# Kernel tuning notes

Measured on AMD Instinct MI355X. Metric: run time of the kernel, lower is better.

Reference implementation:

```python
import jax, jax.numpy as jnp
import numpy as np
from jax import lax

NUM_CAMERAS = 15
INPUT_SIZE = 1024
NUM_TIMESTEPS = 60
BATCH = 256


def setup_inputs() -> dict:
    key = jax.random.key(0)
    k1, k2, k3, k4, k5, k6 = jax.random.split(key, 6)
    H = INPUT_SIZE
    s = 1.0 / np.sqrt(H)  # PyTorch RNNCell init: U(-1/sqrt(H), 1/sqrt(H))
    x = jax.random.normal(k1, (BATCH, H), dtype=jnp.float32)
    cam = jax.random.randint(k2, (BATCH,), 0, NUM_CAMERAS)
    # per-camera GRUCell params, PyTorch layout: gates [r, z, n] stacked -> 3H
    W_ih = jax.random.uniform(k3, (NUM_CAMERAS, 3 * H, H), jnp.float32, -s, s)
    W_hh = jax.random.uniform(k4, (NUM_CAMERAS, 3 * H, H), jnp.float32, -s, s)
    b_ih = jax.random.uniform(k5, (NUM_CAMERAS, 3 * H), jnp.float32, -s, s)
    b_hh = jax.random.uniform(k6, (NUM_CAMERAS, 3 * H), jnp.float32, -s, s)
    return {"x": x, "cam": cam, "W_ih": W_ih, "W_hh": W_hh, "b_ih": b_ih, "b_hh": b_hh}


def reference(x, cam, W_ih, W_hh, b_ih, b_hh):
    B, H = x.shape
    rows = jnp.arange(B)
    # input projection is constant across timesteps (same x fed every step):
    # compute for all cameras as one GEMM, then gather each sample's camera.
    gi_all = jnp.einsum('bh,cgh->bcg', x, W_ih) + b_ih[None]  # [B,C,3H]
    gi = gi_all[rows, cam]                                     # [B,3H]
    gi_r, gi_z, gi_n = jnp.split(gi, 3, axis=1)
    bhh = b_hh[cam]                                            # [B,3H]

    def step(h, _):
        gh_all = jnp.einsum('bh,cgh->bcg', h, W_hh)            # [B,C,3H] GEMM
        gh = gh_all[rows, cam] + bhh                           # [B,3H]
        gh_r, gh_z, gh_n = jnp.split(gh, 3, axis=1)
        r = jax.nn.sigmoid(gi_r + gh_r)
        z = jax.nn.sigmoid(gi_z + gh_z)
        n = jnp.tanh(gi_n + r * gh_n)
        h_new = (1.0 - z) * n + z * h
        return h_new, h_new

    h0 = jnp.zeros((B, H), dtype=x.dtype)
    _, hs = lax.scan(step, h0, None, length=NUM_TIMESTEPS)     # [T,B,H]
    return jnp.transpose(hs, (1, 2, 0))                        # [B,H,T]
```

## Files before the change

### kernel.cpp

```cpp
#include <hip/hip_runtime.h>
#include <math.h>

#define HD 1024
#define BB 256
#define NCAM 15
#define TT 60
#define G3 3072
#define LDW 36
#define NS 24
#define TCH 20

typedef _Float16 f16x8 __attribute__((ext_vector_type(8)));
typedef float f32x4 __attribute__((ext_vector_type(4)));

__device__ __forceinline__ unsigned short f2h(float f) {
    _Float16 h = (_Float16)f;
    unsigned short u;
    __builtin_memcpy(&u, &h, 2);
    return u;
}
__device__ __forceinline__ float sigf(float v) { return 1.f / (1.f + expf(-v)); }

__device__ __forceinline__ void dma16(const void* g, void* l) {
    __builtin_amdgcn_global_load_lds(
        (const __attribute__((address_space(1))) unsigned int*)g,
        (__attribute__((address_space(3))) unsigned int*)l, 16, 0, 0);
}

__global__ void group_kernel(const int* __restrict__ cam,
                             int* __restrict__ off, int* __restrict__ list) {
    __shared__ int cnt[NCAM];
    __shared__ int soff[NCAM + 1];
    int tid = threadIdx.x;
    if (tid < NCAM) cnt[tid] = 0;
    __syncthreads();
    int c = cam[tid];
    int pos = atomicAdd(&cnt[c], 1);
    __syncthreads();
    if (tid == 0) {
        soff[0] = 0;
        for (int i = 0; i < NCAM; ++i) soff[i + 1] = soff[i] + cnt[i];
    }
    __syncthreads();
    list[soff[c] + pos] = tid;
    if (tid <= NCAM) off[tid] = soff[tid];
}

__global__ __launch_bounds__(256) void gi_gemm_kernel(
    const float* __restrict__ W_ih, const float* __restrict__ b_ih,
    const float* __restrict__ b_hh, const float* __restrict__ x,
    const int* __restrict__ off, const int* __restrict__ list,
    float* __restrict__ gi) {
    int c  = blockIdx.x;
    int r0 = blockIdx.y * 96;
    int tid = threadIdx.x;
    int tx = tid & 7, ty = tid >> 3;

    __shared__ __align__(16) float wlds[96 * LDW];
    __shared__ __align__(16) float hlds[NS * LDW];
    __shared__ int slist[NS];

    int base = off[c];
    int nc = off[c + 1] - base;

    for (int s0 = 0; s0 < nc; s0 += NS) {
        __syncthreads();
        if (tid < NS) slist[tid] = (s0 + tid < nc) ? list[base + s0 + tid] : -1;
        __syncthreads();

        float acc[3][3];
#pragma unroll
        for (int g = 0; g < 3; ++g)
#pragma unroll
            for (int q = 0; q < 3; ++q) acc[g][q] = 0.f;

        for (int k0 = 0; k0 < HD; k0 += 32) {
#pragma unroll
            for (int i = 0; i < 3; ++i) {
                int idx = tid + 256 * i;
                int row = idx >> 3, col4 = idx & 7;
                float4 w = *(const float4*)(W_ih +
                    ((size_t)c * G3 + r0 + row) * HD + k0 + col4 * 4);
                *(float4*)(wlds + row * LDW + col4 * 4) = w;
            }
            {
                int s = tid >> 3, col4 = tid & 7;
                if (s < NS) {
                    int b = slist[s];
                    float4 hv = make_float4(0.f, 0.f, 0.f, 0.f);
                    if (b >= 0)
                        hv = *(const float4*)(x + (size_t)b * HD + k0 + col4 * 4);
                    *(float4*)(hlds + s * LDW + col4 * 4) = hv;
                }
            }
            __syncthreads();
#pragma unroll
            for (int kk = 0; kk < 32; kk += 4) {
                float4 w0 = *(const float4*)(wlds + (0 * 32 + ty) * LDW + kk);
                float4 w1 = *(const float4*)(wlds + (1 * 32 + ty) * LDW + kk);
                float4 w2 = *(const float4*)(wlds + (2 * 32 + ty) * LDW + kk);
#pragma unroll
                for (int q = 0; q < 3; ++q) {
                    float4 hv = *(const float4*)(hlds + (tx + 8 * q) * LDW + kk);
                    acc[0][q] += w0.x * hv.x + w0.y * hv.y + w0.z * hv.z + w0.w * hv.w;
                    acc[1][q] += w1.x * hv.x + w1.y * hv.y + w1.z * hv.z + w1.w * hv.w;
                    acc[2][q] += w2.x * hv.x + w2.y * hv.y + w2.z * hv.z + w2.w * hv.w;
                }
            }
            __syncthreads();
        }
#pragma unroll
        for (int q = 0; q < 3; ++q) {
            int b = slist[tx + 8 * q];
            if (b >= 0) {
#pragma unroll
                for (int g = 0; g < 3; ++g) {
                    int R = r0 + g * 32 + ty;
                    float bias = b_ih[c * G3 + R];
                    if (R < 2 * HD) bias += b_hh[c * G3 + R];
                    gi[(size_t)b * G3 + R] = acc[g][q] + bias;
                }
            }
        }
    }
}

__global__ __launch_bounds__(256) void prep_kernel(
    const float* __restrict__ W_hh, unsigned short* __restrict__ Wimg) {
    int c = blockIdx.z, jt = blockIdx.y;
    int lin = blockIdx.x * 256 + threadIdx.x;
    int it  = lin / 768;
    int rem = lin - it * 768;
    int r = rem >> 3, kcp = rem & 7;
    int gate = r >> 5, jl = r & 31;
    int kc = kcp ^ (r & 7);
    int k = it * 64 + kc * 8;
    const float* src = W_hh + ((size_t)c * G3 + gate * HD + jt * 32 + jl) * HD + k;
    float4 v0 = *(const float4*)src;
    float4 v1 = *(const float4*)(src + 4);
    float v[8] = {v0.x, v0.y, v0.z, v0.w, v1.x, v1.y, v1.z, v1.w};
    unsigned int hp[4];
#pragma unroll
    for (int e = 0; e < 4; ++e) {
        unsigned short h0 = f2h(v[2 * e]), h1 = f2h(v[2 * e + 1]);
        hp[e] = (unsigned)h0 | ((unsigned)h1 << 16);
    }
    unsigned short* dst = Wimg + ((size_t)(c * 32 + jt) * 16 + it) * 6144 + r * 64 + kcp * 8;
    *(uint4*)dst = make_uint4(hp[0], hp[1], hp[2], hp[3]);
}

__global__ __launch_bounds__(128) void step_dma_kernel(
    const unsigned short* __restrict__ Wimg, const float* __restrict__ b_hh,
    const float* __restrict__ gi, const int* __restrict__ off,
    const int* __restrict__ list, const float* __restrict__ h_in,
    const unsigned short* __restrict__ hf_in, const unsigned short* __restrict__ hzero,
    float* __restrict__ h_out, unsigned short* __restrict__ hf_out) {
    int c  = blockIdx.x;
    int jt = blockIdx.y;
    int j0 = jt * 32;
    int tid = threadIdx.x;
    int lane = tid & 63;
    int w = tid >> 6;
    int l15 = lane & 15;
    int l4  = lane >> 4;

    __shared__ __align__(16) unsigned short Ash[4][6144];
    __shared__ __align__(16) unsigned short Bsh[4][2048];

    const unsigned short* wbase = Wimg + (size_t)(c * 32 + jt) * 16 * 6144;
    int base = off[c];
    int nc = off[c + 1] - base;

    int bs[2], bkc[2];
#pragma unroll
    for (int i = 0; i < 2; ++i) {
        int p = i * 128 + tid;
        bs[i]  = p >> 3;
        bkc[i] = (p & 7) ^ (bs[i] & 7);
    }

#define STG_A(NB, IT) do {                                                    \
        const char* asrc_ = (const char*)(wbase + (size_t)(IT) * 6144);       \
        _Pragma("unroll")                                                     \
        for (int i_ = 0; i_ < 6; ++i_)                                        \
            dma16(asrc_ + (i_ * 128 + tid) * 16,                              \
                  (char*)(Ash[NB]) + (i_ * 128 + (w << 6)) * 16);             \
    } while (0)
#define STG_B(NB, IT) do {                                                    \
        int k0_ = (IT) * 64;                                                  \
        _Pragma("unroll")                                                     \
        for (int i_ = 0; i_ < 2; ++i_)                                        \
            dma16(bg[i_] + k0_ * bstep[i_],                                   \
                  (char*)(Bsh[NB]) + (i_ * 128 + (w << 6)) * 16);             \
    } while (0)

    for (int s0 = 0; s0 < nc; s0 += 32) {
        __syncthreads();

        int sv = -1;
        if (lane < 32) sv = (s0 + lane < nc) ? list[base + s0 + lane] : -1;

        int rem = nc - s0;
        int nq = (rem > 16) ? 2 : 1;

        const unsigned short* bg[2];
        int bstep[2];
#pragma unroll
        for (int i = 0; i < 2; ++i) {
            int b = __shfl(sv, bs[i]);
            bg[i] = (b >= 0) ? hf_in + (size_t)b * HD + bkc[i] * 8 : hzero;
            bstep[i] = (b >= 0) ? 1 : 0;
        }

        f32x4 acc[3][2];
#pragma unroll
        for (int g = 0; g < 3; ++g)
#pragma unroll
            for (int q = 0; q < 2; ++q) acc[g][q] = (f32x4){0.f, 0.f, 0.f, 0.f};

        asm volatile("s_waitcnt vmcnt(0)" ::: "memory");

        STG_A(0, 0); STG_B(0, 0);
        STG_A(1, 1); STG_B(1, 1);
        STG_A(2, 2); STG_B(2, 2);

#pragma unroll
        for (int it = 0; it < 16; ++it) {
            if (it < 14)       asm volatile("s_waitcnt vmcnt(16)" ::: "memory");
            else if (it == 14) asm volatile("s_waitcnt vmcnt(8)"  ::: "memory");
            else               asm volatile("s_waitcnt vmcnt(0)"  ::: "memory");
            __builtin_amdgcn_s_barrier();
            if (it < 13) { STG_A((it + 3) & 3, it + 3); STG_B((it + 3) & 3, it + 3); }

            const unsigned short* Acur = Ash[it & 3];
            const unsigned short* Bcur = Bsh[it & 3];
#pragma unroll
            for (int kt = 0; kt < 2; ++kt) {
                int kc = kt * 4 + l4;
                f16x8 bq[2];
#pragma unroll
                for (int q = 0; q < 2; ++q) {
                    if (q < nq) {
                        int s = q * 16 + l15;
                        int boff = s * 64 + ((kc ^ (s & 7)) * 8);
                        bq[q] = *(const f16x8*)(&Bcur[boff]);
                    }
                }
#pragma unroll
                for (int g = 0; g < 3; ++g) {
                    int r = g * 32 + w * 16 + l15;
                    int aoff = r * 64 + ((kc ^ (r & 7)) * 8);
                    f16x8 av = *(const f16x8*)(&Acur[aoff]);
#pragma unroll
                    for (int q = 0; q < 2; ++q) {
                        if (q < nq) {
                            acc[g][q] = __builtin_amdgcn_mfma_f32_16x16x32_f16(av, bq[q], acc[g][q], 0, 0, 0);
                        }
                    }
                }
            }
        }

        int j = j0 + w * 16 + l4 * 4;
        f32x4 bhn = *(const f32x4*)(b_hh + c * G3 + 2 * HD + j);
#pragma unroll
        for (int q = 0; q < 2; ++q) {
            if (q < nq) {
                int b = __shfl(sv, q * 16 + l15);
                if (b >= 0) {
                    const float* gib = gi + (size_t)b * G3;
                    f32x4 gr = *(const f32x4*)(gib + j);
                    f32x4 gz = *(const f32x4*)(gib + HD + j);
                    f32x4 gn = *(const f32x4*)(gib + 2 * HD + j);
                    f32x4 hp = *(const f32x4*)(h_in + (size_t)b * HD + j);
                    f32x4 hn;
#pragma unroll
                    for (int e = 0; e < 4; ++e) {
                        float r = sigf(gr[e] + acc[0][q][e]);
                        float z = sigf(gz[e] + acc[1][q][e]);
                        float n = tanhf(gn[e] + r * (acc[2][q][e] + bhn[e]));
                        hn[e] = (1.f - z) * n + z * hp[e];
                    }
                    unsigned int hw[2];
#pragma unroll
                    for (int e = 0; e < 2; ++e) {
                        unsigned short h0 = f2h(hn[2 * e]), h1 = f2h(hn[2 * e + 1]);
                        hw[e] = (unsigned)h0 | ((unsigned)h1 << 16);
                    }
                    *(f32x4*)(h_out + (size_t)b * HD + j) = hn;
                    *(uint2*)(hf_out + (size_t)b * HD + j) = make_uint2(hw[0], hw[1]);
                }
            }
        }
    }
#undef STG_A
#undef STG_B
}

__global__ __launch_bounds__(256) void tr_kernel(
    const float* __restrict__ ring, float* __restrict__ out, int t0) {
    int r = blockIdx.x * 256 + threadIdx.x;
    float v[TCH];
#pragma unroll
    for (int tt = 0; tt < TCH; ++tt)
        v[tt] = ring[(size_t)tt * (BB * HD) + r];
    float* dst = out + (size_t)r * TT + t0;
#pragma unroll
    for (int e = 0; e < TCH / 4; ++e)
        *(f32x4*)(dst + 4 * e) = (f32x4){v[4 * e], v[4 * e + 1], v[4 * e + 2], v[4 * e + 3]};
}

extern "C" void kernel_launch(void* const* d_in, const int* in_sizes, int n_in,
                              void* d_out, int out_size, void* d_ws, size_t ws_size,
                              hipStream_t stream) {
    const float* x    = (const float*)d_in[0];
    const int*   cam  = (const int*)d_in[1];
    const float* W_ih = (const float*)d_in[2];
    const float* W_hh = (const float*)d_in[3];
    const float* b_ih = (const float*)d_in[4];
    const float* b_hh = (const float*)d_in[5];
    float* out = (float*)d_out;

    char* ws = (char*)d_ws;
    int*   off   = (int*)ws;
    int*   list  = (int*)(ws + 64);
    unsigned short* hzero = (unsigned short*)(ws + 2048);
    float* gi    = (float*)(ws + 4096);
    float* hZ    = (float*)(ws + 3149824);
    unsigned short* hfA = (unsigned short*)(ws + 4198400);
    unsigned short* hfB = (unsigned short*)(ws + 4722688);
    float* ring  = (float*)(ws + 5246976);
    unsigned short* Wimg = (unsigned short*)(ws + 26218496);

    group_kernel<<<1, 256, 0, stream>>>(cam, off, list);
    gi_gemm_kernel<<<dim3(NCAM, G3 / 96), 256, 0, stream>>>(
        W_ih, b_ih, b_hh, x, off, list, gi);
    prep_kernel<<<dim3(48, 32, NCAM), 256, 0, stream>>>(W_hh, Wimg);
    hipMemsetAsync(hzero, 0, 2048, stream);
    hipMemsetAsync(hZ, 0, (size_t)BB * HD * sizeof(float), stream);
    hipMemsetAsync(hfA, 0, (size_t)BB * HD * sizeof(short), stream);

    const float* hin = hZ;
    const unsigned short* hf_in = hfA;
    unsigned short* hf_out = hfB;
    for (int t = 0; t < TT; ++t) {
        float* ringplane = ring + (size_t)(t % TCH) * BB * HD;
        step_dma_kernel<<<dim3(NCAM, HD / 32), 128, 0, stream>>>(
            Wimg, b_hh, gi, off, list, hin, hf_in, hzero,
            ringplane, hf_out);
        hin = ringplane;
        { const unsigned short* tmp = hf_in; hf_in = hf_out; hf_out = (unsigned short*)tmp; }
        if ((t % TCH) == TCH - 1)
            tr_kernel<<<BB * HD / 256, 256, 0, stream>>>(ring, out, t - (TCH - 1));
    }
}
```

Measured before the change: 1.743 ms.

## Fuse timesteps into persistent kernel with register-resident weights and per-camera barriers

Replaces the 60 per-step launches and the ring/transpose kernels with one persistent kernel. Each block keeps its FP16 W_hh tile in registers for all timesteps and keeps its fp32 hidden state in registers. Blocks of the same camera sync through an atomic arrival counter, and each block writes its output directly in [B,H,T] layout. This removes the per-step weight restreaming and launch overhead. In exchange it needs very high register pressure with spill risk, relies on all 480 blocks being co-resident, and writes output as strided, uncoalesced stores.

New measurement: 5.755 ms. +230.2%, slower.

```diff
diff --git a/kernel.cpp b/kernel.cpp
--- a/kernel.cpp
+++ b/kernel.cpp
@@ -8,7 +8,6 @@
 #define G3 3072
 #define LDW 36
 #define NS 24
-#define TCH 20
 
 typedef _Float16 f16x8 __attribute__((ext_vector_type(8)));
 typedef float f32x4 __attribute__((ext_vector_type(4)));
@@ -20,12 +19,6 @@
     return u;
 }
 __device__ __forceinline__ float sigf(float v) { return 1.f / (1.f + expf(-v)); }
-
-__device__ __forceinline__ void dma16(const void* g, void* l) {
-    __builtin_amdgcn_global_load_lds(
-        (const __attribute__((address_space(1))) unsigned int*)g,
-        (__attribute__((address_space(3))) unsigned int*)l, 16, 0, 0);
-}
 
 __global__ void group_kernel(const int* __restrict__ cam,
                              int* __restrict__ off, int* __restrict__ list) {
@@ -149,12 +142,12 @@
     *(uint4*)dst = make_uint4(hp[0], hp[1], hp[2], hp[3]);
 }
 
-__global__ __launch_bounds__(128) void step_dma_kernel(
+__global__ __launch_bounds__(128, 1) void persist_kernel(
     const unsigned short* __restrict__ Wimg, const float* __restrict__ b_hh,
     const float* __restrict__ gi, const int* __restrict__ off,
-    const int* __restrict__ list, const float* __restrict__ h_in,
-    const unsigned short* __restrict__ hf_in, const unsigned short* __restrict__ hzero,
-    float* __restrict__ h_out, unsigned short* __restrict__ hf_out) {
+    const int* __restrict__ list, const unsigned short* __restrict__ hzero,
+    unsigned short* __restrict__ hfA, unsigned short* __restrict__ hfB,
+    int* __restrict__ arr, float* __restrict__ out) {
     int c  = blockIdx.x;
     int jt = blockIdx.y;
     int j0 = jt * 32;
@@ -164,150 +157,136 @@
     int l15 = lane & 15;
     int l4  = lane >> 4;
 
-    __shared__ __align__(16) unsigned short Ash[4][6144];
-    __shared__ __align__(16) unsigned short Bsh[4][2048];
-
-    const unsigned short* wbase = Wimg + (size_t)(c * 32 + jt) * 16 * 6144;
+    f16x8 wreg[96];
+    {
+        const unsigned short* wbase = Wimg + (size_t)(c * 32 + jt) * 16 * 6144;
+#pragma unroll
+        for (int it = 0; it < 16; ++it)
+#pragma unroll
+            for (int kt = 0; kt < 2; ++kt)
+#pragma unroll
+                for (int g = 0; g < 3; ++g) {
+                    int r = g * 32 + w * 16 + l15;
+                    int kc = kt * 4 + l4;
+                    int kcp = kc ^ (r & 7);
+                    wreg[(it * 2 + kt) * 3 + g] =
+                        *(const f16x8*)(wbase + (size_t)it * 6144 + r * 64 + kcp * 8);
+                }
+    }
+
     int base = off[c];
     int nc = off[c + 1] - base;
-
-    int bs[2], bkc[2];
-#pragma unroll
-    for (int i = 0; i < 2; ++i) {
-        int p = i * 128 + tid;
-        bs[i]  = p >> 3;
-        bkc[i] = (p & 7) ^ (bs[i] & 7);
-    }
-
-#define STG_A(NB, IT) do {                                                    \
-        const char* asrc_ = (const char*)(wbase + (size_t)(IT) * 6144);       \
-        _Pragma("unroll")                                                     \
-        for (int i_ = 0; i_ < 6; ++i_)                                        \
-            dma16(asrc_ + (i_ * 128 + tid) * 16,                              \
-                  (char*)(Ash[NB]) + (i_ * 128 + (w << 6)) * 16);             \
-    } while (0)
-#define STG_B(NB, IT) do {                                                    \
-        int k0_ = (IT) * 64;                                                  \
-        _Pragma("unroll")                                                     \
-        for (int i_ = 0; i_ < 2; ++i_)                                        \
-            dma16(bg[i_] + k0_ * bstep[i_],                                   \
-                  (char*)(Bsh[NB]) + (i_ * 128 + (w << 6)) * 16);             \
-    } while (0)
-
-    for (int s0 = 0; s0 < nc; s0 += 32) {
-        __syncthreads();
-
-        int sv = -1;
-        if (lane < 32) sv = (s0 + lane < nc) ? list[base + s0 + lane] : -1;
-
-        int rem = nc - s0;
-        int nq = (rem > 16) ? 2 : 1;
-
-        const unsigned short* bg[2];
-        int bstep[2];
-#pragma unroll
-        for (int i = 0; i < 2; ++i) {
-            int b = __shfl(sv, bs[i]);
-            bg[i] = (b >= 0) ? hf_in + (size_t)b * HD + bkc[i] * 8 : hzero;
-            bstep[i] = (b >= 0) ? 1 : 0;
+    int npass = (nc + 31) >> 5;
+
+    f32x4 hreg[2][2];
+#pragma unroll
+    for (int p = 0; p < 2; ++p)
+#pragma unroll
+        for (int q = 0; q < 2; ++q) hreg[p][q] = (f32x4){0.f, 0.f, 0.f, 0.f};
+
+    int j = j0 + w * 16 + l4 * 4;
+    f32x4 bhn = *(const f32x4*)(b_hh + c * G3 + 2 * HD + j);
+    int* arrc = arr + c;
+
+    for (int t = 0; t < TT; ++t) {
+        const unsigned short* hf_in = (t & 1) ? hfB : hfA;
+        unsigned short*      hf_out = (t & 1) ? hfA : hfB;
+
+        if (t) {
+            if (tid == 0) {
+                int target = 32 * t;
+                int guard = 0;
+                while (__hip_atomic_load(arrc, __ATOMIC_RELAXED,
+                                         __HIP_MEMORY_SCOPE_AGENT) < target) {
+                    __builtin_amdgcn_s_sleep(2);
+                    if (++guard > (1 << 20)) break;
+                }
+            }
+            __syncthreads();
+            __threadfence();
         }
 
-        f32x4 acc[3][2];
-#pragma unroll
-        for (int g = 0; g < 3; ++g)
-#pragma unroll
-            for (int q = 0; q < 2; ++q) acc[g][q] = (f32x4){0.f, 0.f, 0.f, 0.f};
-
-        asm volatile("s_waitcnt vmcnt(0)" ::: "memory");
-
-        STG_A(0, 0); STG_B(0, 0);
-        STG_A(1, 1); STG_B(1, 1);
-        STG_A(2, 2); STG_B(2, 2);
-
-#pragma unroll
-        for (int it = 0; it < 16; ++it) {
-            if (it < 14)       asm volatile("s_waitcnt vmcnt(16)" ::: "memory");
-            else if (it == 14) asm volatile("s_waitcnt vmcnt(8)"  ::: "memory");
-            else               asm volatile("s_waitcnt vmcnt(0)"  ::: "memory");
-            __builtin_amdgcn_s_barrier();
-            if (it < 13) { STG_A((it + 3) & 3, it + 3); STG_B((it + 3) & 3, it + 3); }
-
-            const unsigned short* Acur = Ash[it & 3];
-            const unsigned short* Bcur = Bsh[it & 3];
-#pragma unroll
-            for (int kt = 0; kt < 2; ++kt) {
-                int kc = kt * 4 + l4;
-                f16x8 bq[2];
+#pragma unroll
+        for (int p = 0; p < 2; ++p) {
+            if (p < npass) {
+                int s0 = p * 32;
+                int sv = -1;
+                if (lane < 32) sv = (s0 + lane < nc) ? list[base + s0 + lane] : -1;
+                int rem = nc - s0;
+                int nq = (rem > 16) ? 2 : 1;
+
+                int bidx[2];
+                const unsigned short* bq_base[2];
+#pragma unroll
+                for (int q = 0; q < 2; ++q) {
+                    bidx[q] = __shfl(sv, q * 16 + l15);
+                    bq_base[q] = (bidx[q] >= 0) ? hf_in + (size_t)bidx[q] * HD : hzero;
+                }
+
+                f32x4 acc[3][2];
+#pragma unroll
+                for (int g = 0; g < 3; ++g)
+#pragma unroll
+                    for (int q = 0; q < 2; ++q) acc[g][q] = (f32x4){0.f, 0.f, 0.f, 0.f};
+
+#pragma unroll
+                for (int it = 0; it < 16; ++it) {
+#pragma unroll
+                    for (int kt = 0; kt < 2; ++kt) {
+                        int koff = it * 64 + (kt * 4 + l4) * 8;
+                        f16x8 bq[2];
+#pragma unroll
+                        for (int q = 0; q < 2; ++q)
+                            if (q < nq) bq[q] = *(const f16x8*)(bq_base[q] + koff);
+#pragma unroll
+                        for (int g = 0; g < 3; ++g) {
+#pragma unroll
+                            for (int q = 0; q < 2; ++q)
+                                if (q < nq)
+                                    acc[g][q] = __builtin_amdgcn_mfma_f32_16x16x32_f16(
+                                        wreg[(it * 2 + kt) * 3 + g], bq[q], acc[g][q], 0, 0, 0);
+                        }
+                    }
+                }
+
 #pragma unroll
                 for (int q = 0; q < 2; ++q) {
                     if (q < nq) {
-                        int s = q * 16 + l15;
-                        int boff = s * 64 + ((kc ^ (s & 7)) * 8);
-                        bq[q] = *(const f16x8*)(&Bcur[boff]);
-                    }
-                }
-#pragma unroll
-                for (int g = 0; g < 3; ++g) {
-                    int r = g * 32 + w * 16 + l15;
-                    int aoff = r * 64 + ((kc ^ (r & 7)) * 8);
-                    f16x8 av = *(const f16x8*)(&Acur[aoff]);
-#pragma unroll
-                    for (int q = 0; q < 2; ++q) {
-                        if (q < nq) {
-                            acc[g][q] = __builtin_amdgcn_mfma_f32_16x16x32_f16(av, bq[q], acc[g][q], 0, 0, 0);
+                        int b = bidx[q];
+                        if (b >= 0) {
+                            const float* gib = gi + (size_t)b * G3;
+                            f32x4 gr = *(const f32x4*)(gib + j);
+                            f32x4 gz = *(const f32x4*)(gib + HD + j);
+                            f32x4 gn = *(const f32x4*)(gib + 2 * HD + j);
+                            f32x4 hp = hreg[p][q];
+                            f32x4 hn;
+#pragma unroll
+                            for (int e = 0; e < 4; ++e) {
+                                float r = sigf(gr[e] + acc[0][q][e]);
+                                float z = sigf(gz[e] + acc[1][q][e]);
+                                float n = tanhf(gn[e] + r * (acc[2][q][e] + bhn[e]));
+                                hn[e] = (1.f - z) * n + z * hp[e];
+                                out[((size_t)(b * HD + j + e)) * TT + t] = hn[e];
+                            }
+                            hreg[p][q] = hn;
+                            unsigned int hw[2];
+#pragma unroll
+                            for (int e = 0; e < 2; ++e) {
+                                unsigned short h0 = f2h(hn[2 * e]), h1 = f2h(hn[2 * e + 1]);
+                                hw[e] = (unsigned)h0 | ((unsigned)h1 << 16);
+                            }
+                            *(uint2*)(hf_out + (size_t)b * HD + j) = make_uint2(hw[0], hw[1]);
                         }
                     }
                 }
             }
         }
 
-        int j = j0 + w * 16 + l4 * 4;
-        f32x4 bhn = *(const f32x4*)(b_hh + c * G3 + 2 * HD + j);
-#pragma unroll
-        for (int q = 0; q < 2; ++q) {
-            if (q < nq) {
-                int b = __shfl(sv, q * 16 + l15);
-                if (b >= 0) {
-                    const float* gib = gi + (size_t)b * G3;
-                    f32x4 gr = *(const f32x4*)(gib + j);
-                    f32x4 gz = *(const f32x4*)(gib + HD + j);
-                    f32x4 gn = *(const f32x4*)(gib + 2 * HD + j);
-                    f32x4 hp = *(const f32x4*)(h_in + (size_t)b * HD + j);
-                    f32x4 hn;
-#pragma unroll
-                    for (int e = 0; e < 4; ++e) {
-                        float r = sigf(gr[e] + acc[0][q][e]);
-                        float z = sigf(gz[e] + acc[1][q][e]);
-                        float n = tanhf(gn[e] + r * (acc[2][q][e] + bhn[e]));
-                        hn[e] = (1.f - z) * n + z * hp[e];
-                    }
-                    unsigned int hw[2];
-#pragma unroll
-                    for (int e = 0; e < 2; ++e) {
-                        unsigned short h0 = f2h(hn[2 * e]), h1 = f2h(hn[2 * e + 1]);
-                        hw[e] = (unsigned)h0 | ((unsigned)h1 << 16);
-                    }
-                    *(f32x4*)(h_out + (size_t)b * HD + j) = hn;
-                    *(uint2*)(hf_out + (size_t)b * HD + j) = make_uint2(hw[0], hw[1]);
-                }
-            }
-        }
-    }
-#undef STG_A
-#undef STG_B
-}
-
-__global__ __launch_bounds__(256) void tr_kernel(
-    const float* __restrict__ ring, float* __restrict__ out, int t0) {
-    int r = blockIdx.x * 256 + threadIdx.x;
-    float v[TCH];
-#pragma unroll
-    for (int tt = 0; tt < TCH; ++tt)
-        v[tt] = ring[(size_t)tt * (BB * HD) + r];
-    float* dst = out + (size_t)r * TT + t0;
-#pragma unroll
-    for (int e = 0; e < TCH / 4; ++e)
-        *(f32x4*)(dst + 4 * e) = (f32x4){v[4 * e], v[4 * e + 1], v[4 * e + 2], v[4 * e + 3]};
+        __threadfence();
+        __syncthreads();
+        if (tid == 0)
+            __hip_atomic_fetch_add(arrc, 1, __ATOMIC_RELAXED, __HIP_MEMORY_SCOPE_AGENT);
+    }
 }
 
 extern "C" void kernel_launch(void* const* d_in, const int* in_sizes, int n_in,
@@ -324,33 +303,21 @@
     char* ws = (char*)d_ws;
     int*   off   = (int*)ws;
     int*   list  = (int*)(ws + 64);
+    int*   arr   = (int*)(ws + 1088);
     unsigned short* hzero = (unsigned short*)(ws + 2048);
     float* gi    = (float*)(ws + 4096);
-    float* hZ    = (float*)(ws + 3149824);
-    unsigned short* hfA = (unsigned short*)(ws + 4198400);
-    unsigned short* hfB = (unsigned short*)(ws + 4722688);
-    float* ring  = (float*)(ws + 5246976);
-    unsigned short* Wimg = (unsigned short*)(ws + 26218496);
+    unsigned short* hfA = (unsigned short*)(ws + 3149824);
+    unsigned short* hfB = (unsigned short*)(ws + 3674112);
+    unsigned short* Wimg = (unsigned short*)(ws + 4198400);
 
     group_kernel<<<1, 256, 0, stream>>>(cam, off, list);
     gi_gemm_kernel<<<dim3(NCAM, G3 / 96), 256, 0, stream>>>(
         W_ih, b_ih, b_hh, x, off, list, gi);
     prep_kernel<<<dim3(48, 32, NCAM), 256, 0, stream>>>(W_hh, Wimg);
     hipMemsetAsync(hzero, 0, 2048, stream);
-    hipMemsetAsync(hZ, 0, (size_t)BB * HD * sizeof(float), stream);
     hipMemsetAsync(hfA, 0, (size_t)BB * HD * sizeof(short), stream);
-
-    const float* hin = hZ;
-    const unsigned short* hf_in = hfA;
-    unsigned short* hf_out = hfB;
-    for (int t = 0; t < TT; ++t) {
-        float* ringplane = ring + (size_t)(t % TCH) * BB * HD;
-        step_dma_kernel<<<dim3(NCAM, HD / 32), 128, 0, stream>>>(
-            Wimg, b_hh, gi, off, list, hin, hf_in, hzero,
-            ringplane, hf_out);
-        hin = ringplane;
-        { const unsigned short* tmp = hf_in; hf_in = hf_out; hf_out = (unsigned short*)tmp; }
-        if ((t % TCH) == TCH - 1)
-            tr_kernel<<<BB * HD / 256, 256, 0, stream>>>(ring, out, t - (TCH - 1));
-    }
-}
+    hipMemsetAsync(arr, 0, 64, stream);
+
+    persist_kernel<<<dim3(NCAM, HD / 32), 128, 0, stream>>>(
+        Wimg, b_hh, gi, off, list, hzero, hfA, hfB, arr, out);
+}
```
